# Optimization experiments

Measured on AMD Instinct MI355X. Metric: run time of the kernel, lower is better.

The kernel has to match this reference:

```python
import jax, jax.numpy as jnp
import numpy as np
from jax import lax

EPS = 1e-5
K = 32  # k_neighbor

def conv1(x, w):
    # x: [B, Cin, L], w: [Cout, Cin] (1x1 conv, no bias)
    return jnp.einsum('bcl,oc->bol', x, w)

def bn(x, g, b):
    # BatchNorm1d in training mode: batch statistics over (batch, length)
    m = jnp.mean(x, axis=(0, 2), keepdims=True)
    v = jnp.var(x, axis=(0, 2), keepdims=True)
    return g[None, :, None] * (x - m) / jnp.sqrt(v + EPS) + b[None, :, None]

def res_block(x, w1, g1, b1, w2, g2, b2):
    h = jax.nn.gelu(bn(conv1(x, w1), g1, b1), approximate=False)
    h = bn(conv1(h, w2), g2, b2)
    return jax.nn.gelu(h + x, approximate=False)

def extraction(x, conv_w, bn_g, bn_b, fw, fg, fb):
    # conv_w: [n_blocks, 2, C, C]; bn_g/bn_b: [n_blocks, 2, C]
    for i in range(conv_w.shape[0]):
        x = res_block(x, conv_w[i, 0], bn_g[i, 0], bn_b[i, 0],
                      conv_w[i, 1], bn_g[i, 1], bn_b[i, 1])
    # TransformerBlock: ffn (conv+BN) with residual + GELU
    return jax.nn.gelu(x + bn(conv1(x, fw), fg, fb), approximate=False)

def setup_inputs() -> dict:
    key = jax.random.key(0)
    ks = jax.random.split(key, 16)
    B, N, S, C = 8, 4096, 1024, 128  # C = out_channel = 2*channel
    inp = {
        'xyz': jax.random.normal(ks[0], (B, N, 3), dtype=jnp.float32),
        'x': jax.random.normal(ks[1], (B, 64, N), dtype=jnp.float32),
        'fps_idx': jax.random.randint(ks[2], (B, S), 0, N, dtype=jnp.int64),
        'pre_conv_w': jax.random.normal(ks[3], (2, 2, C, C), dtype=jnp.float32) * 0.05,
        'pre_bn_g': jnp.ones((2, 2, C), jnp.float32),
        'pre_bn_b': jnp.zeros((2, 2, C), jnp.float32),
        'pre_ffn_w': jax.random.normal(ks[4], (C, C), dtype=jnp.float32) * 0.05,
        'pre_ffn_g': jnp.ones((C,), jnp.float32),
        'pre_ffn_b': jnp.zeros((C,), jnp.float32),
        'pos_conv_w': jax.random.normal(ks[5], (2, 2, C, C), dtype=jnp.float32) * 0.05,
        'pos_bn_g': jnp.ones((2, 2, C), jnp.float32),
        'pos_bn_b': jnp.zeros((2, 2, C), jnp.float32),
        'pos_ffn_w': jax.random.normal(ks[6], (C, C), dtype=jnp.float32) * 0.05,
        'pos_ffn_g': jnp.ones((C,), jnp.float32),
        'pos_ffn_b': jnp.zeros((C,), jnp.float32),
    }
    return inp

def reference(xyz, x, fps_idx,
              pre_conv_w, pre_bn_g, pre_bn_b, pre_ffn_w, pre_ffn_g, pre_ffn_b,
              pos_conv_w, pos_bn_g, pos_bn_b, pos_ffn_w, pos_ffn_g, pos_ffn_b):
    B, N, _ = xyz.shape
    S = fps_idx.shape[1]
    points = jnp.swapaxes(x, 1, 2)  # [B, N, d]
    d = points.shape[-1]

    # --- LocalGrouper ---
    new_xyz = jnp.take_along_axis(xyz, fps_idx[:, :, None], axis=1)      # [B, S, 3]
    new_pts = jnp.take_along_axis(points, fps_idx[:, :, None], axis=1)  # [B, S, d]

    # squared distances [B, S, N]
    sqr = (jnp.sum(new_xyz ** 2, -1)[:, :, None]
           + jnp.sum(xyz ** 2, -1)[:, None, :]
           - 2.0 * jnp.einsum('bsc,bnc->bsn', new_xyz, xyz))
    idx = lax.top_k(-sqr, K)[1]  # [B, S, K] smallest distances

    grouped = jnp.take_along_axis(points, idx.reshape(B, S * K)[:, :, None],
                                  axis=1).reshape(B, S, K, d)
    center = new_pts[:, :, None, :]  # [B, S, 1, d]
    feat = jnp.concatenate([grouped - center,
                            jnp.broadcast_to(center, grouped.shape)], axis=-1)  # [B,S,K,2d]

    C = 2 * d
    # --- PreExtraction: [B,S,K,C] -> [B*S, C, K] -> maxpool -> [B, C, S] ---
    y = jnp.swapaxes(feat, 2, 3).reshape(B * S, C, K)
    y = extraction(y, pre_conv_w, pre_bn_g, pre_bn_b, pre_ffn_w, pre_ffn_g, pre_ffn_b)
    y = jnp.max(y, axis=-1).reshape(B, S, C)
    y = jnp.swapaxes(y, 1, 2)  # [B, C, S]

    # --- PosExtraction ---
    y = extraction(y, pos_conv_w, pos_bn_g, pos_bn_b, pos_ffn_w, pos_ffn_g, pos_ffn_b)
    return (new_xyz, y)
```

## Files before the change

### kernel.cpp

```cpp
#include <hip/hip_runtime.h>
#include <math.h>

typedef unsigned short ushort_t;
typedef unsigned long long u64;
typedef unsigned int uint32;

#define B_ 8
#define N_ 4096
#define S_ 1024
#define K_ 32
#define C_ 128
#define NCOL1 (B_*S_*K_)
#define NCOL2 (B_*S_)
#define EPS_ 1e-5f

typedef ushort_t us8 __attribute__((ext_vector_type(8)));
typedef short s16x8 __attribute__((ext_vector_type(8)));
typedef float f32x4 __attribute__((ext_vector_type(4)));

__device__ __forceinline__ float bf2f(ushort_t u){ return __uint_as_float(((uint32)u)<<16); }
__device__ __forceinline__ ushort_t f2bf(float f){
    uint32 x = __float_as_uint(f);
    return (ushort_t)((x + 0x7FFFu + ((x>>16)&1u)) >> 16);
}
__device__ __forceinline__ float gelu_f(float v){
    float az = fabsf(v)*0.70710678118654752f;
    float t  = __builtin_amdgcn_rcpf(fmaf(0.3275911f, az, 1.0f));
    float p  = fmaf(fmaf(fmaf(fmaf(1.061405429f, t, -1.453152027f), t, 1.421413741f), t,
                   -0.284496736f), t, 0.254829592f)*t;
    float e  = __expf(-az*az);
    float er = fmaf(-p, e, 1.0f);
    float s  = (v < 0.0f) ? -er : er;
    return 0.5f*v*(1.0f+s);
}
__device__ __forceinline__ u64 shfl_xor_u64(u64 v, int m){
    int lo = __shfl_xor((int)(v & 0xFFFFFFFFull), m, 64);
    int hi = __shfl_xor((int)(v >> 32), m, 64);
    return (((u64)(uint32)hi) << 32) | (uint32)lo;
}
__device__ __forceinline__ void gl_lds16(const char* gp, char* lp){
    __builtin_amdgcn_global_load_lds((const __attribute__((address_space(1))) void*)gp,
                                     (__attribute__((address_space(3))) void*)lp, 16, 0, 0);
}

__global__ __launch_bounds__(256) void transpose_kernel(const float* __restrict__ x, float* __restrict__ xT){
    __shared__ float t[64][65];
    int b  = blockIdx.x >> 6;
    int n0 = (blockIdx.x & 63) * 64;
    int tx = threadIdx.x & 63, ty = threadIdx.x >> 6;
    #pragma unroll
    for (int i=0;i<16;i++){
        int c = i*4 + ty;
        t[c][tx] = x[((long)(b*64 + c))*N_ + n0 + tx];
    }
    __syncthreads();
    #pragma unroll
    for (int i=0;i<16;i++){
        int n = i*4 + ty;
        xT[((long)(b*N_ + n0 + n))*64 + tx] = t[tx][n];
    }
}

__global__ __launch_bounds__(256) void knn_kernel(const float* __restrict__ xyz, const int* __restrict__ fps,
                                                  int* __restrict__ idxg, float* __restrict__ newxyz){
    __shared__ uint32 hist[4096];
    __shared__ u64    cand[1024];
    __shared__ u64    out_keys[64];
    __shared__ uint32 csum[256];
    __shared__ uint32 wtot[4];
    __shared__ uint32 shv[8];
    __shared__ u64    wred[4];
    __shared__ u64    winner;

    int tid = threadIdx.x;
    int wv = tid >> 6, l = tid & 63;
    int bs = blockIdx.x;
    int b  = bs >> 10;
    int qi = fps[bs];
    const float* qb = xyz + ((long)b*N_ + qi)*3;
    float qx = qb[0], qy = qb[1], qz = qb[2];
    if (tid < 3) newxyz[(long)bs*3 + tid] = qb[tid];
    const float* xb = xyz + (long)b*N_*3;

    for (int i=tid;i<1024;i+=256) hist[i]=0;
    if (tid < 8) shv[tid]=0;
    __syncthreads();

    uint32 dbits[16];
    #pragma unroll
    for (int i=0;i<16;i++){
        int n = i*256 + tid;
        float dx = xb[n*3+0]-qx, dy = xb[n*3+1]-qy, dz = xb[n*3+2]-qz;
        float d = dx*dx + dy*dy + dz*dz;
        dbits[i] = __float_as_uint(d);
        atomicAdd(&hist[dbits[i]>>21], 1u);
    }
    __syncthreads();

    {
        uint32 h4[4]; uint32 csumv=0;
        #pragma unroll
        for (int i=0;i<4;i++){ h4[i]=hist[tid*4+i]; csumv+=h4[i]; }
        uint32 sc = csumv;
        #pragma unroll
        for (int off=1; off<64; off<<=1){ uint32 o=__shfl_up(sc,off,64); if (l>=off) sc+=o; }
        if (l==63) wtot[wv]=sc;
        csum[tid]=sc;
        __syncthreads();
        uint32 base=0;
        for (int w2=0; w2<wv; w2++) base += wtot[w2];
        uint32 cum = base + csum[tid] - csumv;
        #pragma unroll
        for (int i=0;i<4;i++){
            if (cum <= 31u && 31u < cum + h4[i]){ shv[0]=(uint32)(tid*4+i); shv[1]=cum; }
            cum += h4[i];
        }
    }
    __syncthreads();
    uint32 b1 = shv[0], cl1 = shv[1];

    for (int i=tid;i<4096;i+=256) hist[i]=0;
    __syncthreads();
    #pragma unroll
    for (int i=0;i<16;i++){
        uint32 u = dbits[i];
        if ((u>>21)==b1) atomicAdd(&hist[(u>>9)&0xFFFu], 1u);
    }
    __syncthreads();

    uint32 r2 = 31u - cl1;
    {
        uint32 h[16]; uint32 csumv=0;
        #pragma unroll
        for (int i=0;i<16;i++){ h[i]=hist[tid*16+i]; csumv += h[i]; }
        uint32 sc = csumv;
        #pragma unroll
        for (int off=1; off<64; off<<=1){ uint32 o=__shfl_up(sc,off,64); if (l>=off) sc+=o; }
        if (l==63) wtot[wv]=sc;
        csum[tid]=sc;
        __syncthreads();
        uint32 base=0;
        for (int w2=0; w2<wv; w2++) base += wtot[w2];
        uint32 cum = base + csum[tid] - csumv;
        #pragma unroll
        for (int i=0;i<16;i++){
            if (cum <= r2 && r2 < cum + h[i]){ shv[2]=(uint32)(tid*16+i); shv[3]=cum; }
            cum += h[i];
        }
    }
    __syncthreads();
    uint32 b2 = shv[2], cl2 = shv[3];
    uint32 nless = cl1 + cl2;

    #pragma unroll
    for (int i=0;i<16;i++){
        uint32 u = dbits[i];
        int n = i*256 + tid;
        uint32 bb1 = u >> 21;
        if (bb1 > b1) continue;
        u64 key = (((u64)u)<<32) | (uint32)n;
        if (bb1 < b1){
            uint32 p = atomicAdd(&shv[4],1u); out_keys[p] = key;
        } else {
            uint32 bb2 = (u>>9)&0xFFFu;
            if (bb2 < b2){ uint32 p = atomicAdd(&shv[4],1u); out_keys[p] = key; }
            else if (bb2 == b2){ uint32 p = atomicAdd(&shv[5],1u); if (p < 1024u) cand[p] = key; }
        }
    }
    __syncthreads();

    if (shv[5] > 1024u){
        uint32 alive = 0xFFFFu;
        for (int r=0;r<K_;r++){
            u64 lmin = ~0ull;
            #pragma unroll
            for (int i=0;i<16;i++){
                u64 k = (((u64)dbits[i])<<32) | (uint32)(i*256+tid);
                if (((alive>>i)&1u) && k < lmin) lmin = k;
            }
            #pragma unroll
            for (int off=32; off>=1; off>>=1){
                u64 o = shfl_xor_u64(lmin, off);
                if (o < lmin) lmin = o;
            }
            if (l == 0) wred[wv] = lmin;
            __syncthreads();
            if (tid == 0){
                u64 m = wred[0];
                if (wred[1]<m) m=wred[1];
                if (wred[2]<m) m=wred[2];
                if (wred[3]<m) m=wred[3];
                winner = m;
                idxg[(long)bs*K_ + r] = (int)(m & 0xFFFFFFFFull);
            }
            __syncthreads();
            u64 w = winner;
            #pragma unroll
            for (int i=0;i<16;i++){
                u64 k = (((u64)dbits[i])<<32) | (uint32)(i*256+tid);
                if (k == w) alive &= ~(1u<<i);
            }
        }
    } else if (wv == 0){
        uint32 cb   = shv[5];
        uint32 need = 32u - nless;
        for (uint32 r=0; r<need; r++){
            u64 lmin = ~0ull;
            for (uint32 s=l; s<cb; s+=64){ u64 kk = cand[s]; if (kk < lmin) lmin = kk; }
            #pragma unroll
            for (int off=32; off>=1; off>>=1){
                u64 o = shfl_xor_u64(lmin, off);
                if (o < lmin) lmin = o;
            }
            for (uint32 s=l; s<cb; s+=64){ if (cand[s]==lmin) cand[s] = ~0ull; }
            if (l==0) out_keys[nless + r] = lmin;
        }
        u64 key = (l < 32) ? out_keys[l] : ~0ull;
        #pragma unroll
        for (uint32 k=2; k<=64; k<<=1){
            bool dir = ((l & k)==0);
            #pragma unroll
            for (uint32 j=k>>1; j>=1; j>>=1){
                u64 o = shfl_xor_u64(key, j);
                bool lower = ((l & j)==0);
                u64 mn = (key < o) ? key : o;
                u64 mx = (key < o) ? o : key;
                key = (lower == dir) ? mn : mx;
            }
        }
        if (l < 32) idxg[(long)bs*K_ + l] = (int)(key & 0xFFFFFFFFull);
    }
}

__global__ __launch_bounds__(256) void build_kernel(const float* __restrict__ xT, const int* __restrict__ fps,
                                                    const int* __restrict__ idxg, ushort_t* __restrict__ A){
    long col = (long)blockIdx.x*256 + threadIdx.x;
    long bs  = col >> 5;
    int  b   = (int)(bs >> 10);
    int  n   = idxg[col];
    int  cn  = fps[bs];
    const float4* pr = (const float4*)(xT + ((long)b*N_ + n )*64);
    const float4* cr = (const float4*)(xT + ((long)b*N_ + cn)*64);
    ushort_t* op = A + col*C_;
    #pragma unroll
    for (int j=0;j<16;j++){
        float4 p = pr[j], c = cr[j];
        uint2 d, e;
        d.x = (((uint32)f2bf(p.y-c.y))<<16) | f2bf(p.x-c.x);
        d.y = (((uint32)f2bf(p.w-c.w))<<16) | f2bf(p.z-c.z);
        e.x = (((uint32)f2bf(c.y))<<16) | f2bf(c.x);
        e.y = (((uint32)f2bf(c.w))<<16) | f2bf(c.z);
        *(uint2*)(op + j*4)      = d;
        *(uint2*)(op + 64 + j*4) = e;
    }
}

__global__ __launch_bounds__(256) void wcvt_kernel(const float* __restrict__ pcw, const float* __restrict__ pfw,
                                                   const float* __restrict__ qcw, const float* __restrict__ qfw,
                                                   ushort_t* __restrict__ Wb){
    int i = blockIdx.x*256 + threadIdx.x;
    int mat = i >> 14;
    int r = i & 16383;
    float v;
    if (mat < 4)      v = pcw[i];
    else if (mat == 4) v = pfw[r];
    else if (mat < 9)  v = qcw[i - 5*16384];
    else               v = qfw[r];
    Wb[i] = f2bf(v);
}

template<int MODE, int PROLOG>
__global__ __launch_bounds__(256) void conv_mfma(const ushort_t* in1, const ushort_t* in2, ushort_t* aux,
                                                 ushort_t* out, const ushort_t* __restrict__ Wb,
                                                 const float* __restrict__ scsh_g, const float* __restrict__ pbprev,
                                                 const float* __restrict__ g, const float* __restrict__ bb,
                                                 float* __restrict__ pb, int nb, float inv_cnt){
    __shared__ ushort_t inT[16384];
    __shared__ float ss[256];
    __shared__ float sL[4][128], qL[4][128];
    int tid = threadIdx.x;
    int w = tid >> 6, l = tid & 63;
    int l15 = l & 15, l4 = l >> 4;

    {
        const char* gt = (const char*)(in1 + (((long)blockIdx.x) << 7)*C_);
        char* lb = (char*)inT;
        #pragma unroll
        for (int i=0;i<8;i++){
            int p = i*4096 + w*1024 + l*16;
            int src = p ^ (((p>>8)&7)<<4);
            gl_lds16(gt + src, lb + i*4096 + w*1024);
        }
    }

    long col0 = ((long)blockIdx.x << 7) + ((long)w << 5);

    s16x8 a2[8];
    if (MODE == 2){
        #pragma unroll
        for (int t=0;t<8;t++){
            int n = t>>2, ks = t&3;
            a2[t] = *(const s16x8*)(in2 + (col0 + n*16 + l15)*C_ + ks*32 + l4*8);
        }
    }

    if (MODE > 0){
        if (PROLOG){
            if (tid < 128){
                const float4* ps = (const float4*)(pbprev + tid*64);
                const float4* pq = (const float4*)(pbprev + (128+tid)*64);
                float s=0.f, q=0.f;
                #pragma unroll
                for (int i=0;i<16;i++){ float4 a=ps[i]; s += (a.x+a.y)+(a.z+a.w); }
                #pragma unroll
                for (int i=0;i<16;i++){ float4 a=pq[i]; q += (a.x+a.y)+(a.z+a.w); }
                float mean = s*inv_cnt, var = q*inv_cnt - mean*mean;
                float sc = g[tid]*rsqrtf(var+EPS_);
                ss[tid*2]   = sc;
                ss[tid*2+1] = bb[tid] - mean*sc;
            }
        } else {
            ss[tid] = scsh_g[tid];
        }
    }
    __syncthreads();

    const char* lb = (const char*)inT;
    f32x4 acc[8][2] = {};
    #pragma unroll
    for (int ks=0; ks<4; ks++){
        int kl = ks*32 + l4*8;
        s16x8 af[8];
        #pragma unroll
        for (int m=0;m<8;m++)
            af[m] = *(const s16x8*)(Wb + (m*16 + l15)*C_ + kl);
        s16x8 bv[2];
        #pragma unroll
        for (int n=0;n<2;n++){
            int colr = (w<<5) + n*16 + l15;
            int boff = (ks*64 + l4*16) ^ ((l15&7)<<4);
            bv[n] = *(const s16x8*)(lb + colr*256 + boff);
        }
        if (MODE > 0){
            float sc[8], sh[8];
            const float4* sp = (const float4*)(&ss[kl*2]);
            float4 s0 = sp[0], s1 = sp[1], s2 = sp[2], s3 = sp[3];
            sc[0]=s0.x; sh[0]=s0.y; sc[1]=s0.z; sh[1]=s0.w;
            sc[2]=s1.x; sh[2]=s1.y; sc[3]=s1.z; sh[3]=s1.w;
            sc[4]=s2.x; sh[4]=s2.y; sc[5]=s2.z; sh[5]=s2.w;
            sc[6]=s3.x; sh[6]=s3.y; sc[7]=s3.z; sh[7]=s3.w;
            #pragma unroll
            for (int n=0;n<2;n++){
                s16x8 v = bv[n];
                if (MODE == 1){
                    #pragma unroll
                    for (int e=0;e<8;e++){
                        float f = gelu_f(fmaf(bf2f((ushort_t)v[e]), sc[e], sh[e]));
                        v[e] = (short)f2bf(f);
                    }
                } else {
                    s16x8 a = a2[n*4+ks];
                    #pragma unroll
                    for (int e=0;e<8;e++){
                        float f = gelu_f(fmaf(bf2f((ushort_t)v[e]), sc[e], sh[e]) + bf2f((ushort_t)a[e]));
                        v[e] = (short)f2bf(f);
                    }
                }
                bv[n] = v;
                if (MODE == 2)
                    *(s16x8*)(aux + (col0 + n*16 + l15)*C_ + kl) = v;
            }
        }
        #pragma unroll
        for (int m=0;m<8;m++)
            #pragma unroll
            for (int n=0;n<2;n++)
                acc[m][n] = __builtin_amdgcn_mfma_f32_16x16x32_bf16(af[m], bv[n], acc[m][n], 0, 0, 0);
    }

    #pragma unroll
    for (int n=0;n<2;n++){
        long cadr = (col0 + n*16 + l15)*C_;
        #pragma unroll
        for (int m=0;m<8;m++){
            f32x4 a = acc[m][n];
            uint2 st;
            st.x = (((uint32)f2bf(a[1]))<<16) | f2bf(a[0]);
            st.y = (((uint32)f2bf(a[3]))<<16) | f2bf(a[2]);
            *(uint2*)(out + cadr + m*16 + l4*4) = st;
        }
    }

    #pragma unroll
    for (int m=0;m<8;m++){
        #pragma unroll
        for (int r=0;r<4;r++){
            float a0=acc[m][0][r], a1=acc[m][1][r];
            float s = a0+a1;
            float q = a0*a0+a1*a1;
            #pragma unroll
            for (int off=1; off<16; off<<=1){
                s += __shfl_xor(s, off, 64);
                q += __shfl_xor(q, off, 64);
            }
            if (l15 == 0){
                sL[w][m*16 + l4*4 + r] = s;
                qL[w][m*16 + l4*4 + r] = q;
            }
        }
    }
    __syncthreads();
    if (tid < 128){
        float s = sL[0][tid] + sL[1][tid] + sL[2][tid] + sL[3][tid];
        float q = qL[0][tid] + qL[1][tid] + qL[2][tid] + qL[3][tid];
        pb[(long)tid*nb + blockIdx.x]       = s;
        pb[(long)(128+tid)*nb + blockIdx.x] = q;
    }
}

__global__ __launch_bounds__(256) void reduce_fin_kernel(const float* __restrict__ pb, float* __restrict__ scsh,
                                                         const float* __restrict__ g, const float* __restrict__ bb,
                                                         float inv_cnt, int nb){
    int oc = blockIdx.x;
    float s=0.f, q=0.f;
    for (int b=threadIdx.x; b<nb; b+=256){
        s += pb[(long)oc*nb + b];
        q += pb[(long)(128+oc)*nb + b];
    }
    __shared__ float ls[256], lq[256];
    ls[threadIdx.x]=s; lq[threadIdx.x]=q;
    __syncthreads();
    #pragma unroll
    for (int st_=128; st_>0; st_>>=1){
        if (threadIdx.x < st_){ ls[threadIdx.x]+=ls[threadIdx.x+st_]; lq[threadIdx.x]+=lq[threadIdx.x+st_]; }
        __syncthreads();
    }
    if (threadIdx.x==0){
        float mean = ls[0]*inv_cnt;
        float var  = lq[0]*inv_cnt - mean*mean;
        float sc   = g[oc]*rsqrtf(var + EPS_);
        scsh[oc*2+0] = sc;
        scsh[oc*2+1] = bb[oc] - mean*sc;
    }
}

__global__ __launch_bounds__(256) void pool_kernel(const ushort_t* __restrict__ T, const ushort_t* __restrict__ X,
                                                   const float* __restrict__ scsh, ushort_t* __restrict__ A2){
    long p  = (long)blockIdx.x*256 + threadIdx.x;
    long bs = p >> 6;
    int  c0 = ((int)p & 63)*2;
    float sc0=scsh[c0*2], sh0=scsh[c0*2+1], sc1=scsh[c0*2+2], sh1=scsh[c0*2+3];
    const ushort_t* tb = T + (bs*K_)*(long)C_ + c0;
    const ushort_t* xv = X + (bs*K_)*(long)C_ + c0;
    float m0 = -1e30f, m1 = -1e30f;
    #pragma unroll 4
    for (int k=0;k<K_;k++){
        uint32 tv = *(const uint32*)(tb + (long)k*C_);
        uint32 av = *(const uint32*)(xv + (long)k*C_);
        float v0 = gelu_f(fmaf(bf2f((ushort_t)(tv & 0xFFFFu)), sc0, sh0) + bf2f((ushort_t)(av & 0xFFFFu)));
        float v1 = gelu_f(fmaf(bf2f((ushort_t)(tv >> 16)),     sc1, sh1) + bf2f((ushort_t)(av >> 16)));
        m0 = fmaxf(m0, v0);
        m1 = fmaxf(m1, v1);
    }
    uint32 o = (((uint32)f2bf(m1))<<16) | f2bf(m0);
    *(uint32*)(A2 + bs*C_ + c0) = o;
}

__global__ __launch_bounds__(256) void out_kernel(const ushort_t* __restrict__ T, const ushort_t* __restrict__ X,
                                                  const float* __restrict__ scsh, float* __restrict__ y){
    long o = (long)blockIdx.x*256 + threadIdx.x;
    int s = (int)(o & (S_-1));
    int c = (int)((o >> 10) & (C_-1));
    int b = (int)(o >> 17);
    long ad = ((long)(b*S_ + s))*C_ + c;
    float v = gelu_f(fmaf(bf2f(T[ad]), scsh[c*2], scsh[c*2+1]) + bf2f(X[ad]));
    y[o] = v;
}

extern "C" void kernel_launch(void* const* d_in, const int* in_sizes, int n_in,
                              void* d_out, int out_size, void* d_ws, size_t ws_size,
                              hipStream_t stream){
    const float* xyz        = (const float*)d_in[0];
    const float* x          = (const float*)d_in[1];
    const int*   fps        = (const int*)d_in[2];
    const float* pre_bn_g   = (const float*)d_in[4];
    const float* pre_bn_b   = (const float*)d_in[5];
    const float* pre_ffn_g  = (const float*)d_in[7];
    const float* pre_ffn_b  = (const float*)d_in[8];
    const float* pos_bn_g   = (const float*)d_in[10];
    const float* pos_bn_b   = (const float*)d_in[11];
    const float* pos_ffn_g  = (const float*)d_in[13];
    const float* pos_ffn_b  = (const float*)d_in[14];

    float* out_xyz = (float*)d_out;
    float* out_y   = (float*)d_out + (long)B_*S_*3;

    char* ws = (char*)d_ws;
    float*    scsh  = (float*)(ws + 0);
    float*    pb2a  = (float*)(ws + 10240);
    float*    pb2b  = (float*)(ws + 75776);
    ushort_t* Wb    = (ushort_t*)(ws + 141312);
    int*      idx   = (int*)(ws + 468992);
    float*    pb    = (float*)(ws + 468992);
    float*    xT    = (float*)(ws + 2566144);
    ushort_t* A2    = (ushort_t*)(ws + 2566144);
    ushort_t* C2    = (ushort_t*)(ws + 4663296);
    ushort_t* A1    = (ushort_t*)(ws + 10954752);
    ushort_t* Cb    = (ushort_t*)(ws + 78063616);
    (void)in_sizes; (void)n_in; (void)out_size; (void)ws_size;

    const float inv1 = 1.0f/(float)NCOL1, inv2 = 1.0f/(float)NCOL2;
    const ushort_t* Wp = Wb;
    const ushort_t* Wq = Wb + 5*C_*C_;

    wcvt_kernel<<<640,256,0,stream>>>((const float*)d_in[3], (const float*)d_in[6],
                                      (const float*)d_in[9], (const float*)d_in[12], Wb);
    transpose_kernel<<<B_*(N_/64),256,0,stream>>>(x, xT);
    knn_kernel<<<B_*S_,256,0,stream>>>(xyz, fps, idx, out_xyz);
    build_kernel<<<NCOL1/256,256,0,stream>>>(xT, fps, idx, A1);

    {
        int nb = NCOL1/128;
        const float* G[5]  = {pre_bn_g, pre_bn_g+C_, pre_bn_g+2*C_, pre_bn_g+3*C_, pre_ffn_g};
        const float* Bv[5] = {pre_bn_b, pre_bn_b+C_, pre_bn_b+2*C_, pre_bn_b+3*C_, pre_ffn_b};
        conv_mfma<0,0><<<nb,256,0,stream>>>(A1, nullptr, nullptr, Cb, Wp+0*C_*C_, nullptr, nullptr, nullptr, nullptr, pb, nb, inv1);
        reduce_fin_kernel<<<128,256,0,stream>>>(pb, scsh+0*256, G[0], Bv[0], inv1, nb);
        conv_mfma<1,0><<<nb,256,0,stream>>>(Cb, nullptr, nullptr, Cb, Wp+1*C_*C_, scsh+0*256, nullptr, nullptr, nullptr, pb, nb, inv1);
        reduce_fin_kernel<<<128,256,0,stream>>>(pb, scsh+1*256, G[1], Bv[1], inv1, nb);
        conv_mfma<2,0><<<nb,256,0,stream>>>(Cb, A1, A1, Cb, Wp+2*C_*C_, scsh+1*256, nullptr, nullptr, nullptr, pb, nb, inv1);
        reduce_fin_kernel<<<128,256,0,stream>>>(pb, scsh+2*256, G[2], Bv[2], inv1, nb);
        conv_mfma<1,0><<<nb,256,0,stream>>>(Cb, nullptr, nullptr, Cb, Wp+3*C_*C_, scsh+2*256, nullptr, nullptr, nullptr, pb, nb, inv1);
        reduce_fin_kernel<<<128,256,0,stream>>>(pb, scsh+3*256, G[3], Bv[3], inv1, nb);
        conv_mfma<2,0><<<nb,256,0,stream>>>(Cb, A1, A1, Cb, Wp+4*C_*C_, scsh+3*256, nullptr, nullptr, nullptr, pb, nb, inv1);
        reduce_fin_kernel<<<128,256,0,stream>>>(pb, scsh+4*256, G[4], Bv[4], inv1, nb);
        pool_kernel<<<(NCOL2*64)/256,256,0,stream>>>(Cb, A1, scsh+4*256, A2);
    }

    {
        int nb = NCOL2/128;
        const float* G[5]  = {pos_bn_g, pos_bn_g+C_, pos_bn_g+2*C_, pos_bn_g+3*C_, pos_ffn_g};
        const float* Bv[5] = {pos_bn_b, pos_bn_b+C_, pos_bn_b+2*C_, pos_bn_b+3*C_, pos_ffn_b};
        conv_mfma<0,1><<<nb,256,0,stream>>>(A2, nullptr, nullptr, C2, Wq+0*C_*C_, nullptr, nullptr, nullptr, nullptr, pb2a, nb, inv2);
        conv_mfma<1,1><<<nb,256,0,stream>>>(C2, nullptr, nullptr, C2, Wq+1*C_*C_, nullptr, pb2a, G[0], Bv[0], pb2b, nb, inv2);
        conv_mfma<2,1><<<nb,256,0,stream>>>(C2, A2, A2, C2, Wq+2*C_*C_, nullptr, pb2b, G[1], Bv[1], pb2a, nb, inv2);
        conv_mfma<1,1><<<nb,256,0,stream>>>(C2, nullptr, nullptr, C2, Wq+3*C_*C_, nullptr, pb2a, G[2], Bv[2], pb2b, nb, inv2);
        conv_mfma<2,1><<<nb,256,0,stream>>>(C2, A2, A2, C2, Wq+4*C_*C_, nullptr, pb2b, G[3], Bv[3], pb2a, nb, inv2);
        reduce_fin_kernel<<<128,256,0,stream>>>(pb2a, scsh+5*256, G[4], Bv[4], inv2, nb);
        out_kernel<<<(B_*C_*S_)/256,256,0,stream>>>(C2, A2, scsh+5*256, out_y);
    }
}
```

Measured before the change: 665.5 us.

## Make conv_mfma persistent with double-buffered LDS tiles and per-wave BN partials

The stage-1 convolutions now run on a fixed grid of 512 blocks, each looping over 4 column tiles. The next tile is prefetched into a second LDS buffer, and its residual operands into registers, while the current tile is computed, with explicit vmcnt waits. Batch-norm partial sums are now written per wave as interleaved (sum, sumsq) pairs instead of through an LDS reduction and __syncthreads, which also changes the reduce kernels and the workspace offsets. The cost is double the LDS use, which may lower occupancy, and four times more partial entries for the reducers to read.

```diff
diff --git a/kernel.cpp b/kernel.cpp
--- a/kernel.cpp
+++ b/kernel.cpp
@@ -42,6 +42,9 @@
     __builtin_amdgcn_global_load_lds((const __attribute__((address_space(1))) void*)gp,
                                      (__attribute__((address_space(3))) void*)lp, 16, 0, 0);
 }
+#define WAITVM(N) do{ __builtin_amdgcn_sched_barrier(0); \
+                      asm volatile("s_waitcnt vmcnt(" #N ")" ::: "memory"); \
+                      __builtin_amdgcn_sched_barrier(0); }while(0)
 
 __global__ __launch_bounds__(256) void transpose_kernel(const float* __restrict__ x, float* __restrict__ xT){
     __shared__ float t[64][65];
@@ -269,51 +272,44 @@
     Wb[i] = f2bf(v);
 }
 
-template<int MODE, int PROLOG>
+template<int MODE, int PROLOG, int NT>
 __global__ __launch_bounds__(256) void conv_mfma(const ushort_t* in1, const ushort_t* in2, ushort_t* aux,
                                                  ushort_t* out, const ushort_t* __restrict__ Wb,
                                                  const float* __restrict__ scsh_g, const float* __restrict__ pbprev,
                                                  const float* __restrict__ g, const float* __restrict__ bb,
-                                                 float* __restrict__ pb, int nb, float inv_cnt){
-    __shared__ ushort_t inT[16384];
+                                                 float* __restrict__ pb, int ntw, float inv_cnt){
+    __shared__ ushort_t inT[2][16384];
     __shared__ float ss[256];
-    __shared__ float sL[4][128], qL[4][128];
     int tid = threadIdx.x;
     int w = tid >> 6, l = tid & 63;
     int l15 = l & 15, l4 = l >> 4;
+    int G = gridDim.x;
 
     {
-        const char* gt = (const char*)(in1 + (((long)blockIdx.x) << 7)*C_);
-        char* lb = (char*)inT;
+        const char* gt = (const char*)in1 + (long)blockIdx.x*32768;
+        char* lbase = (char*)&inT[0][0] + w*8192;
         #pragma unroll
         for (int i=0;i<8;i++){
-            int p = i*4096 + w*1024 + l*16;
+            int p = w*8192 + i*1024 + l*16;
             int src = p ^ (((p>>8)&7)<<4);
-            gl_lds16(gt + src, lb + i*4096 + w*1024);
-        }
-    }
-
-    long col0 = ((long)blockIdx.x << 7) + ((long)w << 5);
-
-    s16x8 a2[8];
+            gl_lds16(gt + src, lbase + i*1024);
+        }
+    }
+    s16x8 a2cur[8], a2nxt[8];
     if (MODE == 2){
+        long c0 = (long)blockIdx.x*128 + w*32;
         #pragma unroll
         for (int t=0;t<8;t++){
             int n = t>>2, ks = t&3;
-            a2[t] = *(const s16x8*)(in2 + (col0 + n*16 + l15)*C_ + ks*32 + l4*8);
-        }
-    }
-
+            a2cur[t] = *(const s16x8*)(in2 + (c0 + n*16 + l15)*C_ + ks*32 + l4*8);
+        }
+    }
     if (MODE > 0){
         if (PROLOG){
             if (tid < 128){
-                const float4* ps = (const float4*)(pbprev + tid*64);
-                const float4* pq = (const float4*)(pbprev + (128+tid)*64);
+                const float4* pp = (const float4*)(pbprev + 2*(long)tid*256);
                 float s=0.f, q=0.f;
-                #pragma unroll
-                for (int i=0;i<16;i++){ float4 a=ps[i]; s += (a.x+a.y)+(a.z+a.w); }
-                #pragma unroll
-                for (int i=0;i<16;i++){ float4 a=pq[i]; q += (a.x+a.y)+(a.z+a.w); }
+                for (int i=0;i<128;i++){ float4 a=pp[i]; s += a.x + a.z; q += a.y + a.w; }
                 float mean = s*inv_cnt, var = q*inv_cnt - mean*mean;
                 float sc = g[tid]*rsqrtf(var+EPS_);
                 ss[tid*2]   = sc;
@@ -325,107 +321,137 @@
     }
     __syncthreads();
 
-    const char* lb = (const char*)inT;
-    f32x4 acc[8][2] = {};
-    #pragma unroll
-    for (int ks=0; ks<4; ks++){
-        int kl = ks*32 + l4*8;
-        s16x8 af[8];
-        #pragma unroll
-        for (int m=0;m<8;m++)
-            af[m] = *(const s16x8*)(Wb + (m*16 + l15)*C_ + kl);
-        s16x8 bv[2];
+    #pragma unroll
+    for (int t=0; t<NT; t++){
+        long tile = (long)t*G + blockIdx.x;
+        if (t+1 < NT){
+            long tnext = tile + G;
+            const char* gt = (const char*)in1 + tnext*32768;
+            char* lbase = (char*)&inT[(t+1)&1][0] + w*8192;
+            #pragma unroll
+            for (int i=0;i<8;i++){
+                int p = w*8192 + i*1024 + l*16;
+                int src = p ^ (((p>>8)&7)<<4);
+                gl_lds16(gt + src, lbase + i*1024);
+            }
+            if (MODE == 2){
+                long c0 = tnext*128 + w*32;
+                #pragma unroll
+                for (int tt=0;tt<8;tt++){
+                    int n = tt>>2, ks = tt&3;
+                    a2nxt[tt] = *(const s16x8*)(in2 + (c0 + n*16 + l15)*C_ + ks*32 + l4*8);
+                }
+            }
+            if (MODE == 2) WAITVM(16); else WAITVM(8);
+        } else {
+            WAITVM(0);
+        }
+
+        const char* lb = (const char*)&inT[t&1][0];
+        long col0 = tile*128 + w*32;
+        f32x4 acc[8][2] = {};
+        #pragma unroll
+        for (int ks=0; ks<4; ks++){
+            int kl = ks*32 + l4*8;
+            s16x8 af[8];
+            #pragma unroll
+            for (int m=0;m<8;m++)
+                af[m] = *(const s16x8*)(Wb + (m*16 + l15)*C_ + kl);
+            s16x8 bv[2];
+            #pragma unroll
+            for (int n=0;n<2;n++){
+                int q = (n*16+l15)*256 + ks*64 + l4*16;
+                int boff = q ^ (((q>>8)&7)<<4);
+                bv[n] = *(const s16x8*)(lb + w*8192 + boff);
+            }
+            if (MODE > 0){
+                float sc[8], sh[8];
+                const float4* sp = (const float4*)(&ss[kl*2]);
+                float4 s0 = sp[0], s1 = sp[1], s2 = sp[2], s3 = sp[3];
+                sc[0]=s0.x; sh[0]=s0.y; sc[1]=s0.z; sh[1]=s0.w;
+                sc[2]=s1.x; sh[2]=s1.y; sc[3]=s1.z; sh[3]=s1.w;
+                sc[4]=s2.x; sh[4]=s2.y; sc[5]=s2.z; sh[5]=s2.w;
+                sc[6]=s3.x; sh[6]=s3.y; sc[7]=s3.z; sh[7]=s3.w;
+                #pragma unroll
+                for (int n=0;n<2;n++){
+                    s16x8 v = bv[n];
+                    if (MODE == 1){
+                        #pragma unroll
+                        for (int e=0;e<8;e++){
+                            float f = gelu_f(fmaf(bf2f((ushort_t)v[e]), sc[e], sh[e]));
+                            v[e] = (short)f2bf(f);
+                        }
+                    } else {
+                        s16x8 a = a2cur[n*4+ks];
+                        #pragma unroll
+                        for (int e=0;e<8;e++){
+                            float f = gelu_f(fmaf(bf2f((ushort_t)v[e]), sc[e], sh[e]) + bf2f((ushort_t)a[e]));
+                            v[e] = (short)f2bf(f);
+                        }
+                    }
+                    bv[n] = v;
+                    if (MODE == 2)
+                        *(s16x8*)(aux + (col0 + n*16 + l15)*C_ + kl) = v;
+                }
+            }
+            #pragma unroll
+            for (int m=0;m<8;m++)
+                #pragma unroll
+                for (int n=0;n<2;n++)
+                    acc[m][n] = __builtin_amdgcn_mfma_f32_16x16x32_bf16(af[m], bv[n], acc[m][n], 0, 0, 0);
+        }
+
         #pragma unroll
         for (int n=0;n<2;n++){
-            int colr = (w<<5) + n*16 + l15;
-            int boff = (ks*64 + l4*16) ^ ((l15&7)<<4);
-            bv[n] = *(const s16x8*)(lb + colr*256 + boff);
-        }
-        if (MODE > 0){
-            float sc[8], sh[8];
-            const float4* sp = (const float4*)(&ss[kl*2]);
-            float4 s0 = sp[0], s1 = sp[1], s2 = sp[2], s3 = sp[3];
-            sc[0]=s0.x; sh[0]=s0.y; sc[1]=s0.z; sh[1]=s0.w;
-            sc[2]=s1.x; sh[2]=s1.y; sc[3]=s1.z; sh[3]=s1.w;
-            sc[4]=s2.x; sh[4]=s2.y; sc[5]=s2.z; sh[5]=s2.w;
-            sc[6]=s3.x; sh[6]=s3.y; sc[7]=s3.z; sh[7]=s3.w;
-            #pragma unroll
-            for (int n=0;n<2;n++){
-                s16x8 v = bv[n];
-                if (MODE == 1){
+            long cadr = (col0 + n*16 + l15)*C_;
+            #pragma unroll
+            for (int m=0;m<8;m++){
+                f32x4 a = acc[m][n];
+                uint2 st;
+                st.x = (((uint32)f2bf(a[1]))<<16) | f2bf(a[0]);
+                st.y = (((uint32)f2bf(a[3]))<<16) | f2bf(a[2]);
+                *(uint2*)(out + cadr + m*16 + l4*4) = st;
+            }
+        }
+
+        {
+            int tw = (int)(tile*4) + w;
+            #pragma unroll
+            for (int m=0;m<8;m++){
+                #pragma unroll
+                for (int r=0;r<4;r++){
+                    float a0=acc[m][0][r], a1=acc[m][1][r];
+                    float s = a0+a1;
+                    float q = a0*a0+a1*a1;
                     #pragma unroll
-                    for (int e=0;e<8;e++){
-                        float f = gelu_f(fmaf(bf2f((ushort_t)v[e]), sc[e], sh[e]));
-                        v[e] = (short)f2bf(f);
+                    for (int off=1; off<16; off<<=1){
+                        s += __shfl_xor(s, off, 64);
+                        q += __shfl_xor(q, off, 64);
                     }
-                } else {
-                    s16x8 a = a2[n*4+ks];
-                    #pragma unroll
-                    for (int e=0;e<8;e++){
-                        float f = gelu_f(fmaf(bf2f((ushort_t)v[e]), sc[e], sh[e]) + bf2f((ushort_t)a[e]));
-                        v[e] = (short)f2bf(f);
+                    if (l15 == m){
+                        int oc = m*16 + l4*4 + r;
+                        float2 v; v.x = s; v.y = q;
+                        *(float2*)(pb + 2*((long)oc*ntw + tw)) = v;
                     }
                 }
-                bv[n] = v;
-                if (MODE == 2)
-                    *(s16x8*)(aux + (col0 + n*16 + l15)*C_ + kl) = v;
-            }
-        }
-        #pragma unroll
-        for (int m=0;m<8;m++)
-            #pragma unroll
-            for (int n=0;n<2;n++)
-                acc[m][n] = __builtin_amdgcn_mfma_f32_16x16x32_bf16(af[m], bv[n], acc[m][n], 0, 0, 0);
-    }
-
-    #pragma unroll
-    for (int n=0;n<2;n++){
-        long cadr = (col0 + n*16 + l15)*C_;
-        #pragma unroll
-        for (int m=0;m<8;m++){
-            f32x4 a = acc[m][n];
-            uint2 st;
-            st.x = (((uint32)f2bf(a[1]))<<16) | f2bf(a[0]);
-            st.y = (((uint32)f2bf(a[3]))<<16) | f2bf(a[2]);
-            *(uint2*)(out + cadr + m*16 + l4*4) = st;
-        }
-    }
-
-    #pragma unroll
-    for (int m=0;m<8;m++){
-        #pragma unroll
-        for (int r=0;r<4;r++){
-            float a0=acc[m][0][r], a1=acc[m][1][r];
-            float s = a0+a1;
-            float q = a0*a0+a1*a1;
-            #pragma unroll
-            for (int off=1; off<16; off<<=1){
-                s += __shfl_xor(s, off, 64);
-                q += __shfl_xor(q, off, 64);
-            }
-            if (l15 == 0){
-                sL[w][m*16 + l4*4 + r] = s;
-                qL[w][m*16 + l4*4 + r] = q;
-            }
-        }
-    }
-    __syncthreads();
-    if (tid < 128){
-        float s = sL[0][tid] + sL[1][tid] + sL[2][tid] + sL[3][tid];
-        float q = qL[0][tid] + qL[1][tid] + qL[2][tid] + qL[3][tid];
-        pb[(long)tid*nb + blockIdx.x]       = s;
-        pb[(long)(128+tid)*nb + blockIdx.x] = q;
+            }
+        }
+
+        if (MODE == 2 && t+1 < NT){
+            #pragma unroll
+            for (int tt=0;tt<8;tt++) a2cur[tt] = a2nxt[tt];
+        }
     }
 }
 
 __global__ __launch_bounds__(256) void reduce_fin_kernel(const float* __restrict__ pb, float* __restrict__ scsh,
                                                          const float* __restrict__ g, const float* __restrict__ bb,
-                                                         float inv_cnt, int nb){
+                                                         float inv_cnt, int ntw){
     int oc = blockIdx.x;
     float s=0.f, q=0.f;
-    for (int b=threadIdx.x; b<nb; b+=256){
-        s += pb[(long)oc*nb + b];
-        q += pb[(long)(128+oc)*nb + b];
+    for (int b=threadIdx.x; b<ntw; b+=256){
+        float2 v = *(const float2*)(pb + 2*((long)oc*ntw + b));
+        s += v.x; q += v.y;
     }
     __shared__ float ls[256], lq[256];
     ls[threadIdx.x]=s; lq[threadIdx.x]=q;
@@ -498,11 +524,11 @@
     char* ws = (char*)d_ws;
     float*    scsh  = (float*)(ws + 0);
     float*    pb2a  = (float*)(ws + 10240);
-    float*    pb2b  = (float*)(ws + 75776);
-    ushort_t* Wb    = (ushort_t*)(ws + 141312);
-    int*      idx   = (int*)(ws + 468992);
-    float*    pb    = (float*)(ws + 468992);
+    float*    pb2b  = (float*)(ws + 272384);
+    ushort_t* Wb    = (ushort_t*)(ws + 534528);
+    int*      idx   = (int*)(ws + 862208);
     float*    xT    = (float*)(ws + 2566144);
+    float*    pb1   = (float*)(ws + 2566144);
     ushort_t* A2    = (ushort_t*)(ws + 2566144);
     ushort_t* C2    = (ushort_t*)(ws + 4663296);
     ushort_t* A1    = (ushort_t*)(ws + 10954752);
@@ -512,6 +538,8 @@
     const float inv1 = 1.0f/(float)NCOL1, inv2 = 1.0f/(float)NCOL2;
     const ushort_t* Wp = Wb;
     const ushort_t* Wq = Wb + 5*C_*C_;
+    const int G1 = 512, NTW1 = 2048*4;
+    const int G2 = 64,  NTW2 = 64*4;
 
     wcvt_kernel<<<640,256,0,stream>>>((const float*)d_in[3], (const float*)d_in[6],
                                       (const float*)d_in[9], (const float*)d_in[12], Wb);
@@ -520,32 +548,30 @@
     build_kernel<<<NCOL1/256,256,0,stream>>>(xT, fps, idx, A1);
 
     {
-        int nb = NCOL1/128;
         const float* G[5]  = {pre_bn_g, pre_bn_g+C_, pre_bn_g+2*C_, pre_bn_g+3*C_, pre_ffn_g};
         const float* Bv[5] = {pre_bn_b, pre_bn_b+C_, pre_bn_b+2*C_, pre_bn_b+3*C_, pre_ffn_b};
-        conv_mfma<0,0><<<nb,256,0,stream>>>(A1, nullptr, nullptr, Cb, Wp+0*C_*C_, nullptr, nullptr, nullptr, nullptr, pb, nb, inv1);
-        reduce_fin_kernel<<<128,256,0,stream>>>(pb, scsh+0*256, G[0], Bv[0], inv1, nb);
-        conv_mfma<1,0><<<nb,256,0,stream>>>(Cb, nullptr, nullptr, Cb, Wp+1*C_*C_, scsh+0*256, nullptr, nullptr, nullptr, pb, nb, inv1);
-        reduce_fin_kernel<<<128,256,0,stream>>>(pb, scsh+1*256, G[1], Bv[1], inv1, nb);
-        conv_mfma<2,0><<<nb,256,0,stream>>>(Cb, A1, A1, Cb, Wp+2*C_*C_, scsh+1*256, nullptr, nullptr, nullptr, pb, nb, inv1);
-        reduce_fin_kernel<<<128,256,0,stream>>>(pb, scsh+2*256, G[2], Bv[2], inv1, nb);
-        conv_mfma<1,0><<<nb,256,0,stream>>>(Cb, nullptr, nullptr, Cb, Wp+3*C_*C_, scsh+2*256, nullptr, nullptr, nullptr, pb, nb, inv1);
-        reduce_fin_kernel<<<128,256,0,stream>>>(pb, scsh+3*256, G[3], Bv[3], inv1, nb);
-        conv_mfma<2,0><<<nb,256,0,stream>>>(Cb, A1, A1, Cb, Wp+4*C_*C_, scsh+3*256, nullptr, nullptr, nullptr, pb, nb, inv1);
-        reduce_fin_kernel<<<128,256,0,stream>>>(pb, scsh+4*256, G[4], Bv[4], inv1, nb);
+        conv_mfma<0,0,4><<<G1,256,0,stream>>>(A1, nullptr, nullptr, Cb, Wp+0*C_*C_, nullptr, nullptr, nullptr, nullptr, pb1, NTW1, inv1);
+        reduce_fin_kernel<<<128,256,0,stream>>>(pb1, scsh+0*256, G[0], Bv[0], inv1, NTW1);
+        conv_mfma<1,0,4><<<G1,256,0,stream>>>(Cb, nullptr, nullptr, Cb, Wp+1*C_*C_, scsh+0*256, nullptr, nullptr, nullptr, pb1, NTW1, inv1);
+        reduce_fin_kernel<<<128,256,0,stream>>>(pb1, scsh+1*256, G[1], Bv[1], inv1, NTW1);
+        conv_mfma<2,0,4><<<G1,256,0,stream>>>(Cb, A1, A1, Cb, Wp+2*C_*C_, scsh+1*256, nullptr, nullptr, nullptr, pb1, NTW1, inv1);
+        reduce_fin_kernel<<<128,256,0,stream>>>(pb1, scsh+2*256, G[2], Bv[2], inv1, NTW1);
+        conv_mfma<1,0,4><<<G1,256,0,stream>>>(Cb, nullptr, nullptr, Cb, Wp+3*C_*C_, scsh+2*256, nullptr, nullptr, nullptr, pb1, NTW1, inv1);
+        reduce_fin_kernel<<<128,256,0,stream>>>(pb1, scsh+3*256, G[3], Bv[3], inv1, NTW1);
+        conv_mfma<2,0,4><<<G1,256,0,stream>>>(Cb, A1, A1, Cb, Wp+4*C_*C_, scsh+3*256, nullptr, nullptr, nullptr, pb1, NTW1, inv1);
+        reduce_fin_kernel<<<128,256,0,stream>>>(pb1, scsh+4*256, G[4], Bv[4], inv1, NTW1);
         pool_kernel<<<(NCOL2*64)/256,256,0,stream>>>(Cb, A1, scsh+4*256, A2);
     }
 
     {
-        int nb = NCOL2/128;
         const float* G[5]  = {pos_bn_g, pos_bn_g+C_, pos_bn_g+2*C_, pos_bn_g+3*C_, pos_ffn_g};
         const float* Bv[5] = {pos_bn_b, pos_bn_b+C_, pos_bn_b+2*C_, pos_bn_b+3*C_, pos_ffn_b};
-        conv_mfma<0,1><<<nb,256,0,stream>>>(A2, nullptr, nullptr, C2, Wq+0*C_*C_, nullptr, nullptr, nullptr, nullptr, pb2a, nb, inv2);
-        conv_mfma<1,1><<<nb,256,0,stream>>>(C2, nullptr, nullptr, C2, Wq+1*C_*C_, nullptr, pb2a, G[0], Bv[0], pb2b, nb, inv2);
-        conv_mfma<2,1><<<nb,256,0,stream>>>(C2, A2, A2, C2, Wq+2*C_*C_, nullptr, pb2b, G[1], Bv[1], pb2a, nb, inv2);
-        conv_mfma<1,1><<<nb,256,0,stream>>>(C2, nullptr, nullptr, C2, Wq+3*C_*C_, nullptr, pb2a, G[2], Bv[2], pb2b, nb, inv2);
-        conv_mfma<2,1><<<nb,256,0,stream>>>(C2, A2, A2, C2, Wq+4*C_*C_, nullptr, pb2b, G[3], Bv[3], pb2a, nb, inv2);
-        reduce_fin_kernel<<<128,256,0,stream>>>(pb2a, scsh+5*256, G[4], Bv[4], inv2, nb);
+        conv_mfma<0,1,1><<<G2,256,0,stream>>>(A2, nullptr, nullptr, C2, Wq+0*C_*C_, nullptr, nullptr, nullptr, nullptr, pb2a, NTW2, inv2);
+        conv_mfma<1,1,1><<<G2,256,0,stream>>>(C2, nullptr, nullptr, C2, Wq+1*C_*C_, nullptr, pb2a, G[0], Bv[0], pb2b, NTW2, inv2);
+        conv_mfma<2,1,1><<<G2,256,0,stream>>>(C2, A2, A2, C2, Wq+2*C_*C_, nullptr, pb2b, G[1], Bv[1], pb2a, NTW2, inv2);
+        conv_mfma<1,1,1><<<G2,256,0,stream>>>(C2, nullptr, nullptr, C2, Wq+3*C_*C_, nullptr, pb2a, G[2], Bv[2], pb2b, NTW2, inv2);
+        conv_mfma<2,1,1><<<G2,256,0,stream>>>(C2, A2, A2, C2, Wq+4*C_*C_, nullptr, pb2b, G[3], Bv[3], pb2a, NTW2, inv2);
+        reduce_fin_kernel<<<128,256,0,stream>>>(pb2a, scsh+5*256, G[4], Bv[4], inv2, NTW2);
         out_kernel<<<(B_*C_*S_)/256,256,0,stream>>>(C2, A2, scsh+5*256, out_y);
     }
 }
```

After: 827.3 us. 24.3% more time.
